# Kernel optimization log

Measured on AMD Instinct MI355X. Metric: run time of the kernel, lower is better.

Reference implementation:

```python
import jax, jax.numpy as jnp
import numpy as np

K = 500        # conv kernel == stride (non-overlapping windows)
C_IN = 8       # embedding dim
C_OUT = 128    # conv out channels
VOCAB = 257    # 256 byte values + padding idx 256


def setup_inputs() -> dict:
    key = jax.random.key(0)
    ks = jax.random.split(key, 10)
    B, L = 8, 1 << 20
    x = jax.random.randint(ks[0], (B, L), 0, VOCAB, dtype=jnp.int32)
    emb = 0.1 * jax.random.normal(ks[1], (VOCAB, C_IN), jnp.float32)
    emb = emb.at[VOCAB - 1].set(0.0)  # padding_idx=256 -> zero row
    lim_c = 1.0 / np.sqrt(C_IN * K)
    w1 = jax.random.uniform(ks[2], (C_OUT, C_IN, K), jnp.float32, -lim_c, lim_c)
    b1 = jax.random.uniform(ks[3], (C_OUT,), jnp.float32, -lim_c, lim_c)
    w2 = jax.random.uniform(ks[4], (C_OUT, C_IN, K), jnp.float32, -lim_c, lim_c)
    b2 = jax.random.uniform(ks[5], (C_OUT,), jnp.float32, -lim_c, lim_c)
    lim_d = 1.0 / np.sqrt(C_OUT)
    wd1 = jax.random.uniform(ks[6], (C_OUT, C_OUT), jnp.float32, -lim_d, lim_d)
    bd1 = jax.random.uniform(ks[7], (C_OUT,), jnp.float32, -lim_d, lim_d)
    wd2 = jax.random.uniform(ks[8], (1, C_OUT), jnp.float32, -lim_d, lim_d)
    bd2 = jax.random.uniform(ks[9], (1,), jnp.float32, -lim_d, lim_d)
    return {"x": x, "emb": emb, "w1": w1, "b1": b1, "w2": w2, "b2": b2,
            "wd1": wd1, "bd1": bd1, "wd2": wd2, "bd2": bd2}


def reference(x, emb, w1, b1, w2, b2, wd1, bd1, wd2, bd2):
    B, L = x.shape
    T = (L - K) // K + 1  # valid conv output length (== L // K here)
    xe = emb[x]                                  # [B, L, 8]  embedding lookup
    win = xe[:, : T * K].reshape(B, T, K, C_IN)  # [B, T, 500, 8] non-overlap windows
    c1 = jnp.einsum('btke,oek->bto', win, w1) + b1  # [B, T, 128]
    c2 = jnp.einsum('btke,oek->bto', win, w2) + b2
    gated = jax.nn.relu(c1) * jax.nn.sigmoid(c2)    # gated activation
    pooled = jnp.max(gated, axis=1)                 # global max pool over time -> [B, 128]
    h = jax.nn.relu(pooled @ wd1.T + bd1)           # [B, 128]
    out = jax.nn.sigmoid(h @ wd2.T + bd2)           # [B, 1]
    return out
```

## Files before the change

### kernel.cpp

```cpp
#include <hip/hip_runtime.h>

#define BATCH   8
#define LSEQ    1048576
#define KCONV   500
#define TWIN    2097
#define MROWS   16776
#define KDIM    4000
#define NDIM    256
#define COUT    128
#define VOCAB   257
#define VOCABP  256

#define BMR     80
#define NTILE   210
#define SLABP   20
#define NSLAB   25
#define NG      125
#define PLANE   (NDIM * 32)
#define AROWSH  168
#define STAGEN  (BMR * SLABP)

#define WTF_OFF   0ull
#define WTF_BYTES ((size_t)NG * PLANE * 2)
#define POOL_OFF  (WTF_OFF + WTF_BYTES)

typedef __attribute__((ext_vector_type(8))) __bf16 bf16x8;
typedef __attribute__((ext_vector_type(4))) float  floatx4;

__device__ inline unsigned short f2bf(float f) {
    union { float f; unsigned u; } c; c.f = f;
    return (unsigned short)((c.u + 0x7FFFu + ((c.u >> 16) & 1u)) >> 16);
}
__device__ inline unsigned pack2(float lo, float hi) {
    return (unsigned)f2bf(lo) | ((unsigned)f2bf(hi) << 16);
}

#define LDS_BARRIER() asm volatile("s_waitcnt lgkmcnt(0)\n\ts_barrier" ::: "memory")

__global__ __launch_bounds__(256) void wprep_kernel(const float* __restrict__ w1,
                                                    const float* __restrict__ w2,
                                                    unsigned short* __restrict__ Wtf,
                                                    float* __restrict__ pool) {
    const int n   = blockIdx.x;
    const int tid = threadIdx.x;
    __shared__ float tile[KDIM];
    const float* src = (n < COUT) ? (w1 + (size_t)n * KDIM)
                                  : (w2 + (size_t)(n - COUT) * KDIM);
    for (int i = tid; i < KDIM; i += 256) tile[i] = src[i];
    __syncthreads();
    for (int i = tid; i < KDIM; i += 256) {
        int g = i >> 5, kk = i & 31;
        Wtf[(size_t)g * PLANE + n * 32 + kk] = f2bf(tile[(i & 7) * KCONV + (i >> 3)]);
    }
    if (n == 0 && tid < BATCH * COUT / 2)
        ((float2*)pool)[tid] = float2{0.f, 0.f};
}

__global__ __launch_bounds__(512) void gemm_kernel(const int* __restrict__ x,
                                                   const float* __restrict__ emb,
                                                   const unsigned short* __restrict__ Wtf,
                                                   const float* __restrict__ b1,
                                                   const float* __restrict__ b2,
                                                   float* __restrict__ pool) {
    __shared__ unsigned short tableL[VOCAB * 8];
    __shared__ unsigned short As[2][BMR * AROWSH];

    const int tid  = threadIdx.x;
    const int lane = tid & 63;
    const int wv   = tid >> 6;
    const int m0   = blockIdx.x * BMR;
    const int r16  = lane & 15;
    const int q    = lane >> 4;

    if (tid < VOCAB) {
        const float4* er = (const float4*)(emb + tid * 8);
        float4 a = er[0], b = er[1];
        uint4 u;
        u.x = pack2(a.x, a.y); u.y = pack2(a.z, a.w);
        u.z = pack2(b.x, b.y); u.w = pack2(b.z, b.w);
        *(uint4*)(tableL + tid * 8) = u;
    }

    const int* xptr[4];
    int        loff[4];
    bool       sval[4];
#pragma unroll
    for (int l = 0; l < 4; ++l) {
        int idx = tid + 512 * l;
        sval[l] = (idx < STAGEN);
        int ic  = sval[l] ? idx : 0;
        int row = ic / SLABP;
        int pos = ic - row * SLABP;
        int am  = m0 + row;
        bool av = sval[l] && (am < MROWS);
        sval[l] = av;
        int amc = av ? am : 0;
        int b   = amc / TWIN;
        int t   = amc - b * TWIN;
        xptr[l] = x + ((size_t)b * LSEQ + (size_t)t * KCONV + pos);
        loff[l] = row * AROWSH + pos * 8;
    }

    const int o = wv * 16 + r16;
    const size_t boff0 = (size_t)o * 32 + q * 8;
    const size_t boff1 = (size_t)(o + 128) * 32 + q * 8;

    floatx4 acc[5][2];
#pragma unroll
    for (int i = 0; i < 5; ++i) { acc[i][0] = floatx4{0,0,0,0}; acc[i][1] = floatx4{0,0,0,0}; }

    int xv[4], xn[4];
#pragma unroll
    for (int l = 0; l < 4; ++l) xv[l] = sval[l] ? xptr[l][0] : VOCABP;
    __syncthreads();

#pragma unroll
    for (int l = 0; l < 4; ++l) {
        if (l == 3 && tid >= STAGEN - 3 * 512) break;
        uint4 g = *(const uint4*)(tableL + xv[l] * 8);
        *(uint4*)((unsigned short*)As + loff[l]) = g;
    }
#pragma unroll
    for (int l = 0; l < 4; ++l) xv[l] = sval[l] ? xptr[l][SLABP] : VOCABP;
    LDS_BARRIER();

    bf16x8 bc0[2], bc1[2], bc2[2] = {};
    bc0[0] = *(const bf16x8*)(Wtf + boff0);
    bc0[1] = *(const bf16x8*)(Wtf + boff1);
    bc1[0] = *(const bf16x8*)(Wtf + PLANE + boff0);
    bc1[1] = *(const bf16x8*)(Wtf + PLANE + boff1);

    int buf = 0;
    for (int s = 0; s < NSLAB; ++s) {
        if (s + 2 < NSLAB) {
#pragma unroll
            for (int l = 0; l < 4; ++l)
                xn[l] = sval[l] ? xptr[l][(s + 2) * SLABP] : VOCABP;
        }

        const unsigned short* Asb = (const unsigned short*)As + buf * (BMR * AROWSH);
#pragma unroll
        for (int kt = 0; kt < 5; ++kt) {
            const int g = s * 5 + kt;
            if (g + 2 < NG) {
                const unsigned short* Wp = Wtf + (size_t)(g + 2) * PLANE;
                bc2[0] = *(const bf16x8*)(Wp + boff0);
                bc2[1] = *(const bf16x8*)(Wp + boff1);
            }
            bf16x8 af[5];
#pragma unroll
            for (int i = 0; i < 5; ++i)
                af[i] = *(const bf16x8*)(Asb + (i * 16 + r16) * AROWSH + (kt * 4 + q) * 8);
#pragma unroll
            for (int i = 0; i < 5; ++i) {
                acc[i][0] = __builtin_amdgcn_mfma_f32_16x16x32_bf16(af[i], bc0[0], acc[i][0], 0, 0, 0);
                acc[i][1] = __builtin_amdgcn_mfma_f32_16x16x32_bf16(af[i], bc0[1], acc[i][1], 0, 0, 0);
            }
            bc0[0] = bc1[0]; bc0[1] = bc1[1];
            bc1[0] = bc2[0]; bc1[1] = bc2[1];
        }

        if (s + 1 < NSLAB) {
            unsigned short* d = (unsigned short*)As + (buf ^ 1) * (BMR * AROWSH);
#pragma unroll
            for (int l = 0; l < 4; ++l) {
                if (l == 3 && tid >= STAGEN - 3 * 512) break;
                uint4 g = *(const uint4*)(tableL + xv[l] * 8);
                *(uint4*)(d + loff[l]) = g;
            }
        }
#pragma unroll
        for (int l = 0; l < 4; ++l) xv[l] = xn[l];
        LDS_BARRIER();
        buf ^= 1;
    }

    const float b1v = b1[o], b2v = b2[o];
    float cur = 0.0f;
    int curb  = (m0 + q * 4) / TWIN;
#pragma unroll
    for (int i = 0; i < 5; ++i) {
#pragma unroll
        for (int rg = 0; rg < 4; ++rg) {
            const int row = m0 + i * 16 + q * 4 + rg;
            if (row < MROWS) {
                const int bb = row / TWIN;
                if (bb != curb) {
                    atomicMax((int*)&pool[curb * COUT + o], __float_as_int(cur));
                    cur = 0.0f; curb = bb;
                }
                const float c1 = acc[i][0][rg] + b1v;
                const float c2 = acc[i][1][rg] + b2v;
                const float g  = fmaxf(c1, 0.0f) / (1.0f + __expf(-c2));
                cur = fmaxf(cur, g);
            }
        }
    }
    atomicMax((int*)&pool[curb * COUT + o], __float_as_int(cur));
}

__global__ __launch_bounds__(128) void head_kernel(const float* __restrict__ pool,
                                                   const float* __restrict__ wd1,
                                                   const float* __restrict__ bd1,
                                                   const float* __restrict__ wd2,
                                                   const float* __restrict__ bd2,
                                                   float* __restrict__ out) {
    __shared__ float red[BATCH][COUT];
    int j = threadIdx.x;
    float wj = wd2[j];
#pragma unroll
    for (int b = 0; b < BATCH; ++b) {
        float s = bd1[j];
        for (int i = 0; i < COUT; ++i) s += pool[b * COUT + i] * wd1[j * COUT + i];
        red[b][j] = fmaxf(s, 0.0f) * wj;
    }
    __syncthreads();
    if (j < BATCH) {
        float s = 0.0f;
        for (int i = 0; i < COUT; ++i) s += red[j][i];
        out[j] = 1.0f / (1.0f + expf(-(s + bd2[0])));
    }
}

extern "C" void kernel_launch(void* const* d_in, const int* in_sizes, int n_in,
                              void* d_out, int out_size, void* d_ws, size_t ws_size,
                              hipStream_t stream) {
    const int*   x   = (const int*)d_in[0];
    const float* emb = (const float*)d_in[1];
    const float* w1  = (const float*)d_in[2];
    const float* b1  = (const float*)d_in[3];
    const float* w2  = (const float*)d_in[4];
    const float* b2  = (const float*)d_in[5];
    const float* wd1 = (const float*)d_in[6];
    const float* bd1 = (const float*)d_in[7];
    const float* wd2 = (const float*)d_in[8];
    const float* bd2 = (const float*)d_in[9];
    float* out = (float*)d_out;

    unsigned short* Wtf  = (unsigned short*)((char*)d_ws + WTF_OFF);
    float*          pool = (float*)((char*)d_ws + POOL_OFF);

    wprep_kernel<<<dim3(NDIM), dim3(256), 0, stream>>>(w1, w2, Wtf, pool);
    gemm_kernel<<<dim3(NTILE), dim3(512), 0, stream>>>(x, emb, Wtf, b1, b2, pool);
    head_kernel<<<dim3(1), dim3(128), 0, stream>>>(pool, wd1, bd1, wd2, bd2, out);
}
```

Before: 172.6 us.

## Split GEMM rows over a larger grid with uneven 2- or 3-tile blocks

Replaces the 210-block grid of 80-row tiles with 512 blocks, each covering 2 or 3 sixteen-row tiles (487 blocks take 2, the last 25 take 3), so all 1049 tiles are covered. The LDS staging buffers and per-thread staging slots shrink to match, and launch bounds request 4 blocks per CU. The aim is to fill all CUs on the MI355X (256 CUs) instead of leaving many idle, and to gain occupancy for latency hiding. The cost is that each block re-reads the full weight matrix for fewer rows, raising weight traffic per row, and the loops now carry runtime tile-count checks.

```diff
diff --git a/kernel.cpp b/kernel.cpp
--- a/kernel.cpp
+++ b/kernel.cpp
@@ -11,14 +11,15 @@
 #define VOCAB   257
 #define VOCABP  256
 
-#define BMR     80
-#define NTILE   210
+#define GRID    512
+#define G2BLK   487
+#define MAXT    3
+#define MAXROWS (MAXT * 16)
 #define SLABP   20
 #define NSLAB   25
 #define NG      125
 #define PLANE   (NDIM * 32)
 #define AROWSH  168
-#define STAGEN  (BMR * SLABP)
 
 #define WTF_OFF   0ull
 #define WTF_BYTES ((size_t)NG * PLANE * 2)
@@ -56,21 +57,27 @@
         ((float2*)pool)[tid] = float2{0.f, 0.f};
 }
 
-__global__ __launch_bounds__(512) void gemm_kernel(const int* __restrict__ x,
-                                                   const float* __restrict__ emb,
-                                                   const unsigned short* __restrict__ Wtf,
-                                                   const float* __restrict__ b1,
-                                                   const float* __restrict__ b2,
-                                                   float* __restrict__ pool) {
+__global__ __launch_bounds__(512, 4) void gemm_kernel(const int* __restrict__ x,
+                                                      const float* __restrict__ emb,
+                                                      const unsigned short* __restrict__ Wtf,
+                                                      const float* __restrict__ b1,
+                                                      const float* __restrict__ b2,
+                                                      float* __restrict__ pool) {
     __shared__ unsigned short tableL[VOCAB * 8];
-    __shared__ unsigned short As[2][BMR * AROWSH];
+    __shared__ unsigned short As[2][MAXROWS * AROWSH];
 
     const int tid  = threadIdx.x;
     const int lane = tid & 63;
     const int wv   = tid >> 6;
-    const int m0   = blockIdx.x * BMR;
     const int r16  = lane & 15;
     const int q    = lane >> 4;
+
+    const int bid  = blockIdx.x;
+    int base, nt;
+    if (bid < G2BLK) { base = 2 * bid;                nt = 2; }
+    else             { base = 974 + 3 * (bid - G2BLK); nt = 3; }
+    const int m0     = base * 16;
+    const int stagen = nt * 16 * SLABP;
 
     if (tid < VOCAB) {
         const float4* er = (const float4*)(emb + tid * 8);
@@ -81,20 +88,20 @@
         *(uint4*)(tableL + tid * 8) = u;
     }
 
-    const int* xptr[4];
-    int        loff[4];
-    bool       sval[4];
-#pragma unroll
-    for (int l = 0; l < 4; ++l) {
+    const int* xptr[2];
+    int        loff[2];
+    bool       sval[2];
+#pragma unroll
+    for (int l = 0; l < 2; ++l) {
         int idx = tid + 512 * l;
-        sval[l] = (idx < STAGEN);
-        int ic  = sval[l] ? idx : 0;
+        bool v  = (idx < stagen);
+        int ic  = v ? idx : 0;
         int row = ic / SLABP;
         int pos = ic - row * SLABP;
         int am  = m0 + row;
-        bool av = sval[l] && (am < MROWS);
-        sval[l] = av;
-        int amc = av ? am : 0;
+        v = v && (am < MROWS);
+        sval[l] = v;
+        int amc = v ? am : 0;
         int b   = amc / TWIN;
         int t   = amc - b * TWIN;
         xptr[l] = x + ((size_t)b * LSEQ + (size_t)t * KCONV + pos);
@@ -105,23 +112,24 @@
     const size_t boff0 = (size_t)o * 32 + q * 8;
     const size_t boff1 = (size_t)(o + 128) * 32 + q * 8;
 
-    floatx4 acc[5][2];
-#pragma unroll
-    for (int i = 0; i < 5; ++i) { acc[i][0] = floatx4{0,0,0,0}; acc[i][1] = floatx4{0,0,0,0}; }
-
-    int xv[4], xn[4];
-#pragma unroll
-    for (int l = 0; l < 4; ++l) xv[l] = sval[l] ? xptr[l][0] : VOCABP;
+    floatx4 acc[MAXT][2];
+#pragma unroll
+    for (int i = 0; i < MAXT; ++i) { acc[i][0] = floatx4{0,0,0,0}; acc[i][1] = floatx4{0,0,0,0}; }
+
+    int xv[2], xn[2];
+#pragma unroll
+    for (int l = 0; l < 2; ++l) xv[l] = sval[l] ? xptr[l][0] : VOCABP;
     __syncthreads();
 
 #pragma unroll
-    for (int l = 0; l < 4; ++l) {
-        if (l == 3 && tid >= STAGEN - 3 * 512) break;
-        uint4 g = *(const uint4*)(tableL + xv[l] * 8);
-        *(uint4*)((unsigned short*)As + loff[l]) = g;
-    }
-#pragma unroll
-    for (int l = 0; l < 4; ++l) xv[l] = sval[l] ? xptr[l][SLABP] : VOCABP;
+    for (int l = 0; l < 2; ++l) {
+        if (sval[l]) {
+            uint4 g = *(const uint4*)(tableL + xv[l] * 8);
+            *(uint4*)((unsigned short*)As + loff[l]) = g;
+        }
+    }
+#pragma unroll
+    for (int l = 0; l < 2; ++l) xv[l] = sval[l] ? xptr[l][SLABP] : VOCABP;
     LDS_BARRIER();
 
     bf16x8 bc0[2], bc1[2], bc2[2] = {};
@@ -134,11 +142,11 @@
     for (int s = 0; s < NSLAB; ++s) {
         if (s + 2 < NSLAB) {
 #pragma unroll
-            for (int l = 0; l < 4; ++l)
+            for (int l = 0; l < 2; ++l)
                 xn[l] = sval[l] ? xptr[l][(s + 2) * SLABP] : VOCABP;
         }
 
-        const unsigned short* Asb = (const unsigned short*)As + buf * (BMR * AROWSH);
+        const unsigned short* Asb = (const unsigned short*)As + buf * (MAXROWS * AROWSH);
 #pragma unroll
         for (int kt = 0; kt < 5; ++kt) {
             const int g = s * 5 + kt;
@@ -147,30 +155,33 @@
                 bc2[0] = *(const bf16x8*)(Wp + boff0);
                 bc2[1] = *(const bf16x8*)(Wp + boff1);
             }
-            bf16x8 af[5];
-#pragma unroll
-            for (int i = 0; i < 5; ++i)
-                af[i] = *(const bf16x8*)(Asb + (i * 16 + r16) * AROWSH + (kt * 4 + q) * 8);
-#pragma unroll
-            for (int i = 0; i < 5; ++i) {
-                acc[i][0] = __builtin_amdgcn_mfma_f32_16x16x32_bf16(af[i], bc0[0], acc[i][0], 0, 0, 0);
-                acc[i][1] = __builtin_amdgcn_mfma_f32_16x16x32_bf16(af[i], bc0[1], acc[i][1], 0, 0, 0);
-            }
+            bf16x8 af[MAXT];
+#pragma unroll
+            for (int i = 0; i < MAXT; ++i)
+                if (i < nt)
+                    af[i] = *(const bf16x8*)(Asb + (i * 16 + r16) * AROWSH + (kt * 4 + q) * 8);
+#pragma unroll
+            for (int i = 0; i < MAXT; ++i)
+                if (i < nt) {
+                    acc[i][0] = __builtin_amdgcn_mfma_f32_16x16x32_bf16(af[i], bc0[0], acc[i][0], 0, 0, 0);
+                    acc[i][1] = __builtin_amdgcn_mfma_f32_16x16x32_bf16(af[i], bc0[1], acc[i][1], 0, 0, 0);
+                }
             bc0[0] = bc1[0]; bc0[1] = bc1[1];
             bc1[0] = bc2[0]; bc1[1] = bc2[1];
         }
 
         if (s + 1 < NSLAB) {
-            unsigned short* d = (unsigned short*)As + (buf ^ 1) * (BMR * AROWSH);
-#pragma unroll
-            for (int l = 0; l < 4; ++l) {
-                if (l == 3 && tid >= STAGEN - 3 * 512) break;
-                uint4 g = *(const uint4*)(tableL + xv[l] * 8);
-                *(uint4*)(d + loff[l]) = g;
+            unsigned short* d = (unsigned short*)As + (buf ^ 1) * (MAXROWS * AROWSH);
+#pragma unroll
+            for (int l = 0; l < 2; ++l) {
+                if (sval[l]) {
+                    uint4 g = *(const uint4*)(tableL + xv[l] * 8);
+                    *(uint4*)(d + loff[l]) = g;
+                }
             }
         }
 #pragma unroll
-        for (int l = 0; l < 4; ++l) xv[l] = xn[l];
+        for (int l = 0; l < 2; ++l) xv[l] = xn[l];
         LDS_BARRIER();
         buf ^= 1;
     }
@@ -179,20 +190,22 @@
     float cur = 0.0f;
     int curb  = (m0 + q * 4) / TWIN;
 #pragma unroll
-    for (int i = 0; i < 5; ++i) {
-#pragma unroll
-        for (int rg = 0; rg < 4; ++rg) {
-            const int row = m0 + i * 16 + q * 4 + rg;
-            if (row < MROWS) {
-                const int bb = row / TWIN;
-                if (bb != curb) {
-                    atomicMax((int*)&pool[curb * COUT + o], __float_as_int(cur));
-                    cur = 0.0f; curb = bb;
+    for (int i = 0; i < MAXT; ++i) {
+        if (i < nt) {
+#pragma unroll
+            for (int rg = 0; rg < 4; ++rg) {
+                const int row = m0 + i * 16 + q * 4 + rg;
+                if (row < MROWS) {
+                    const int bb = row / TWIN;
+                    if (bb != curb) {
+                        atomicMax((int*)&pool[curb * COUT + o], __float_as_int(cur));
+                        cur = 0.0f; curb = bb;
+                    }
+                    const float c1 = acc[i][0][rg] + b1v;
+                    const float c2 = acc[i][1][rg] + b2v;
+                    const float g  = fmaxf(c1, 0.0f) / (1.0f + __expf(-c2));
+                    cur = fmaxf(cur, g);
                 }
-                const float c1 = acc[i][0][rg] + b1v;
-                const float c2 = acc[i][1][rg] + b2v;
-                const float g  = fmaxf(c1, 0.0f) / (1.0f + __expf(-c2));
-                cur = fmaxf(cur, g);
             }
         }
     }
@@ -241,6 +254,6 @@
     float*          pool = (float*)((char*)d_ws + POOL_OFF);
 
     wprep_kernel<<<dim3(NDIM), dim3(256), 0, stream>>>(w1, w2, Wtf, pool);
-    gemm_kernel<<<dim3(NTILE), dim3(512), 0, stream>>>(x, emb, Wtf, b1, b2, pool);
+    gemm_kernel<<<dim3(GRID), dim3(512), 0, stream>>>(x, emb, Wtf, b1, b2, pool);
     head_kernel<<<dim3(1), dim3(128), 0, stream>>>(pool, wd1, bd1, wd2, bd2, out);
 }
```

Result: slower. 197.2 us (+14.2%).

## Split wave tiling into 2x4 grid to cut B-fragment global loads

Applied to the files above, without the earlier changes.

Changes the per-wave tile from 80 rows by 32 columns (5 row tiles, 2 column tiles) to a 2x4 wave grid. Each wave now owns 2 or 3 row tiles and 4 column tiles, with the two wave groups splitting the 5 row tiles unevenly (3 and 2). Each weight fragment fetched from global memory is now reused across more MFMAs, and fewer A fragments are read from LDS per wave. The cost is unequal work between the wave groups and more accumulator and B-prefetch registers (12 accumulators, 12 prefetched fragments), which could lower occupancy.

```diff
diff --git a/kernel.cpp b/kernel.cpp
--- a/kernel.cpp
+++ b/kernel.cpp
@@ -72,6 +72,11 @@
     const int r16  = lane & 15;
     const int q    = lane >> 4;
 
+    const int wg   = wv >> 2;
+    const int wn   = wv & 3;
+    const int ntw  = wg ? 2 : 3;
+    const int tb   = wg * 3;
+
     if (tid < VOCAB) {
         const float4* er = (const float4*)(emb + tid * 8);
         float4 a = er[0], b = er[1];
@@ -101,13 +106,14 @@
         loff[l] = row * AROWSH + pos * 8;
     }
 
-    const int o = wv * 16 + r16;
-    const size_t boff0 = (size_t)o * 32 + q * 8;
-    const size_t boff1 = (size_t)(o + 128) * 32 + q * 8;
-
-    floatx4 acc[5][2];
-#pragma unroll
-    for (int i = 0; i < 5; ++i) { acc[i][0] = floatx4{0,0,0,0}; acc[i][1] = floatx4{0,0,0,0}; }
+    const size_t bb0 = (size_t)(wn * 32 + r16) * 32 + q * 8;
+    const size_t boff[4] = { bb0, bb0 + 16 * 32, bb0 + 128 * 32, bb0 + 144 * 32 };
+
+    floatx4 acc[3][4];
+#pragma unroll
+    for (int i = 0; i < 3; ++i)
+#pragma unroll
+        for (int j = 0; j < 4; ++j) acc[i][j] = floatx4{0.f, 0.f, 0.f, 0.f};
 
     int xv[4], xn[4];
 #pragma unroll
@@ -124,11 +130,12 @@
     for (int l = 0; l < 4; ++l) xv[l] = sval[l] ? xptr[l][SLABP] : VOCABP;
     LDS_BARRIER();
 
-    bf16x8 bc0[2], bc1[2], bc2[2] = {};
-    bc0[0] = *(const bf16x8*)(Wtf + boff0);
-    bc0[1] = *(const bf16x8*)(Wtf + boff1);
-    bc1[0] = *(const bf16x8*)(Wtf + PLANE + boff0);
-    bc1[1] = *(const bf16x8*)(Wtf + PLANE + boff1);
+    bf16x8 bc0[4], bc1[4], bc2[4] = {};
+#pragma unroll
+    for (int j = 0; j < 4; ++j) {
+        bc0[j] = *(const bf16x8*)(Wtf + boff[j]);
+        bc1[j] = *(const bf16x8*)(Wtf + PLANE + boff[j]);
+    }
 
     int buf = 0;
     for (int s = 0; s < NSLAB; ++s) {
@@ -144,20 +151,23 @@
             const int g = s * 5 + kt;
             if (g + 2 < NG) {
                 const unsigned short* Wp = Wtf + (size_t)(g + 2) * PLANE;
-                bc2[0] = *(const bf16x8*)(Wp + boff0);
-                bc2[1] = *(const bf16x8*)(Wp + boff1);
+#pragma unroll
+                for (int j = 0; j < 4; ++j) bc2[j] = *(const bf16x8*)(Wp + boff[j]);
             }
-            bf16x8 af[5];
-#pragma unroll
-            for (int i = 0; i < 5; ++i)
-                af[i] = *(const bf16x8*)(Asb + (i * 16 + r16) * AROWSH + (kt * 4 + q) * 8);
-#pragma unroll
-            for (int i = 0; i < 5; ++i) {
-                acc[i][0] = __builtin_amdgcn_mfma_f32_16x16x32_bf16(af[i], bc0[0], acc[i][0], 0, 0, 0);
-                acc[i][1] = __builtin_amdgcn_mfma_f32_16x16x32_bf16(af[i], bc0[1], acc[i][1], 0, 0, 0);
-            }
-            bc0[0] = bc1[0]; bc0[1] = bc1[1];
-            bc1[0] = bc2[0]; bc1[1] = bc2[1];
+            bf16x8 af[3];
+#pragma unroll
+            for (int i = 0; i < 3; ++i)
+                if (i < ntw)
+                    af[i] = *(const bf16x8*)(Asb + ((tb + i) * 16 + r16) * AROWSH + (kt * 4 + q) * 8);
+#pragma unroll
+            for (int i = 0; i < 3; ++i)
+                if (i < ntw) {
+#pragma unroll
+                    for (int j = 0; j < 4; ++j)
+                        acc[i][j] = __builtin_amdgcn_mfma_f32_16x16x32_bf16(af[i], bc0[j], acc[i][j], 0, 0, 0);
+                }
+#pragma unroll
+            for (int j = 0; j < 4; ++j) { bc0[j] = bc1[j]; bc1[j] = bc2[j]; }
         }
 
         if (s + 1 < NSLAB) {
@@ -175,28 +185,34 @@
         buf ^= 1;
     }
 
-    const float b1v = b1[o], b2v = b2[o];
-    float cur = 0.0f;
-    int curb  = (m0 + q * 4) / TWIN;
-#pragma unroll
-    for (int i = 0; i < 5; ++i) {
-#pragma unroll
-        for (int rg = 0; rg < 4; ++rg) {
-            const int row = m0 + i * 16 + q * 4 + rg;
-            if (row < MROWS) {
-                const int bb = row / TWIN;
-                if (bb != curb) {
-                    atomicMax((int*)&pool[curb * COUT + o], __float_as_int(cur));
-                    cur = 0.0f; curb = bb;
+#pragma unroll
+    for (int jj = 0; jj < 2; ++jj) {
+        const int o = wn * 32 + jj * 16 + r16;
+        const float b1v = b1[o], b2v = b2[o];
+        float cur = 0.0f;
+        int curb  = (m0 + tb * 16 + q * 4) / TWIN;
+#pragma unroll
+        for (int i = 0; i < 3; ++i) {
+            if (i < ntw) {
+#pragma unroll
+                for (int rg = 0; rg < 4; ++rg) {
+                    const int row = m0 + (tb + i) * 16 + q * 4 + rg;
+                    if (row < MROWS) {
+                        const int bb = row / TWIN;
+                        if (bb != curb) {
+                            atomicMax((int*)&pool[curb * COUT + o], __float_as_int(cur));
+                            cur = 0.0f; curb = bb;
+                        }
+                        const float c1 = acc[i][jj][rg] + b1v;
+                        const float c2 = acc[i][jj + 2][rg] + b2v;
+                        const float g  = fmaxf(c1, 0.0f) / (1.0f + __expf(-c2));
+                        cur = fmaxf(cur, g);
+                    }
                 }
-                const float c1 = acc[i][0][rg] + b1v;
-                const float c2 = acc[i][1][rg] + b2v;
-                const float g  = fmaxf(c1, 0.0f) / (1.0f + __expf(-c2));
-                cur = fmaxf(cur, g);
             }
         }
-    }
-    atomicMax((int*)&pool[curb * COUT + o], __float_as_int(cur));
+        atomicMax((int*)&pool[curb * COUT + o], __float_as_int(cur));
+    }
 }
 
 __global__ __launch_bounds__(128) void head_kernel(const float* __restrict__ pool,
```

Result: slower. 181.4 us (+5.1%).

## Process A slabs in pairs with four LDS buffers to halve barriers

Applied to the files above, without the earlier changes.

The main loop now handles two K-slabs per iteration, using four LDS staging buffers instead of two. It prefetches x indices four and five slabs ahead and runs a single barrier per pair, so the block synchronizes half as often. The trailing odd slab (24) is computed after the loop from buffer 0. This doubles LDS use for A staging, which may lower occupancy, and raises register pressure from the extra prefetched indices.

```diff
diff --git a/kernel.cpp b/kernel.cpp
--- a/kernel.cpp
+++ b/kernel.cpp
@@ -15,9 +15,11 @@
 #define NTILE   210
 #define SLABP   20
 #define NSLAB   25
+#define NPAIR   12
 #define NG      125
 #define PLANE   (NDIM * 32)
 #define AROWSH  168
+#define SLAB    (BMR * AROWSH)
 #define STAGEN  (BMR * SLABP)
 
 #define WTF_OFF   0ull
@@ -63,7 +65,7 @@
                                                    const float* __restrict__ b2,
                                                    float* __restrict__ pool) {
     __shared__ unsigned short tableL[VOCAB * 8];
-    __shared__ unsigned short As[2][BMR * AROWSH];
+    __shared__ unsigned short As[4][SLAB];
 
     const int tid  = threadIdx.x;
     const int lane = tid & 63;
@@ -109,36 +111,17 @@
 #pragma unroll
     for (int i = 0; i < 5; ++i) { acc[i][0] = floatx4{0,0,0,0}; acc[i][1] = floatx4{0,0,0,0}; }
 
-    int xv[4], xn[4];
-#pragma unroll
-    for (int l = 0; l < 4; ++l) xv[l] = sval[l] ? xptr[l][0] : VOCABP;
-    __syncthreads();
-
-#pragma unroll
-    for (int l = 0; l < 4; ++l) {
-        if (l == 3 && tid >= STAGEN - 3 * 512) break;
-        uint4 g = *(const uint4*)(tableL + xv[l] * 8);
-        *(uint4*)((unsigned short*)As + loff[l]) = g;
-    }
-#pragma unroll
-    for (int l = 0; l < 4; ++l) xv[l] = sval[l] ? xptr[l][SLABP] : VOCABP;
-    LDS_BARRIER();
-
     bf16x8 bc0[2], bc1[2], bc2[2] = {};
-    bc0[0] = *(const bf16x8*)(Wtf + boff0);
-    bc0[1] = *(const bf16x8*)(Wtf + boff1);
-    bc1[0] = *(const bf16x8*)(Wtf + PLANE + boff0);
-    bc1[1] = *(const bf16x8*)(Wtf + PLANE + boff1);
-
-    int buf = 0;
-    for (int s = 0; s < NSLAB; ++s) {
-        if (s + 2 < NSLAB) {
-#pragma unroll
-            for (int l = 0; l < 4; ++l)
-                xn[l] = sval[l] ? xptr[l][(s + 2) * SLABP] : VOCABP;
-        }
-
-        const unsigned short* Asb = (const unsigned short*)As + buf * (BMR * AROWSH);
+
+    auto stage = [&](unsigned short* dst, const int* xs) {
+#pragma unroll
+        for (int l = 0; l < 4; ++l) {
+            if (l == 3 && tid >= STAGEN - 3 * 512) break;
+            uint4 g = *(const uint4*)(tableL + xs[l] * 8);
+            *(uint4*)(dst + loff[l]) = g;
+        }
+    };
+    auto compute_slab = [&](const unsigned short* Asb, int s) {
 #pragma unroll
         for (int kt = 0; kt < 5; ++kt) {
             const int g = s * 5 + kt;
@@ -159,21 +142,53 @@
             bc0[0] = bc1[0]; bc0[1] = bc1[1];
             bc1[0] = bc2[0]; bc1[1] = bc2[1];
         }
-
-        if (s + 1 < NSLAB) {
-            unsigned short* d = (unsigned short*)As + (buf ^ 1) * (BMR * AROWSH);
-#pragma unroll
-            for (int l = 0; l < 4; ++l) {
-                if (l == 3 && tid >= STAGEN - 3 * 512) break;
-                uint4 g = *(const uint4*)(tableL + xv[l] * 8);
-                *(uint4*)(d + loff[l]) = g;
-            }
-        }
-#pragma unroll
-        for (int l = 0; l < 4; ++l) xv[l] = xn[l];
+    };
+
+    int xs0[4], xs1[4], xn0[4], xn1[4];
+#pragma unroll
+    for (int l = 0; l < 4; ++l) {
+        xs0[l] = sval[l] ? xptr[l][0] : VOCABP;
+        xs1[l] = sval[l] ? xptr[l][SLABP] : VOCABP;
+    }
+    __syncthreads();
+
+    stage(&As[0][0], xs0);
+    stage(&As[1][0], xs1);
+#pragma unroll
+    for (int l = 0; l < 4; ++l) {
+        xs0[l] = sval[l] ? xptr[l][2 * SLABP] : VOCABP;
+        xs1[l] = sval[l] ? xptr[l][3 * SLABP] : VOCABP;
+    }
+    LDS_BARRIER();
+
+    bc0[0] = *(const bf16x8*)(Wtf + boff0);
+    bc0[1] = *(const bf16x8*)(Wtf + boff1);
+    bc1[0] = *(const bf16x8*)(Wtf + PLANE + boff0);
+    bc1[1] = *(const bf16x8*)(Wtf + PLANE + boff1);
+
+    for (int p = 0; p < NPAIR; ++p) {
+        const int s0 = 2 * p;
+        if (s0 + 4 < NSLAB) {
+#pragma unroll
+            for (int l = 0; l < 4; ++l) xn0[l] = sval[l] ? xptr[l][(s0 + 4) * SLABP] : VOCABP;
+        }
+        if (s0 + 5 < NSLAB) {
+#pragma unroll
+            for (int l = 0; l < 4; ++l) xn1[l] = sval[l] ? xptr[l][(s0 + 5) * SLABP] : VOCABP;
+        }
+
+        const int half = (p & 1) * 2;
+        compute_slab(&As[half][0],     s0);
+        compute_slab(&As[half + 1][0], s0 + 1);
+
+        const int oh = ((p & 1) ^ 1) * 2;
+        if (s0 + 2 < NSLAB) stage(&As[oh][0],     xs0);
+        if (s0 + 3 < NSLAB) stage(&As[oh + 1][0], xs1);
+#pragma unroll
+        for (int l = 0; l < 4; ++l) { xs0[l] = xn0[l]; xs1[l] = xn1[l]; }
         LDS_BARRIER();
-        buf ^= 1;
-    }
+    }
+    compute_slab(&As[0][0], 24);
 
     const float b1v = b1[o], b2v = b2[o];
     float cur = 0.0f;
```

Result: no change. 170.2 us (-1.4%).
